# Optimization experiments

Hardware: AMD Instinct MI355X
Metric: run time of the kernel (lower is better)

## Reference

```python
import jax, jax.numpy as jnp
import numpy as np

SLOPE = 25.0  # surrogate gradient slope of ALIFNeuron
EPS = 1e-5    # LayerNorm eps


def spike_fn(u):
    # forward: heaviside(u); backward: sigmoid surrogate with slope SLOPE
    s = jax.nn.sigmoid(SLOPE * u)
    hard = (u > 0).astype(u.dtype)
    return s + jax.lax.stop_gradient(hard - s)


def layernorm(x, w, b):
    mu = jnp.mean(x, axis=-1, keepdims=True)
    var = jnp.mean((x - mu) ** 2, axis=-1, keepdims=True)
    return (x - mu) * jax.lax.rsqrt(var + EPS) * w + b


def setup_inputs() -> dict:
    key = jax.random.key(0)
    k1, k2, k3 = jax.random.split(key, 3)
    B, T, D = 8, 4096, 1024
    num_nodes = 15  # (1 << 4) - 1
    x = jax.random.normal(k1, (B, T, D), dtype=jnp.float32)
    # Linear(2D -> D) weights for each tree node, scaled ~ 1/sqrt(fan_in)
    W = jax.random.normal(k2, (num_nodes, 2 * D, D), dtype=jnp.float32) * 0.02
    b = jnp.zeros((num_nodes, D), dtype=jnp.float32)
    # base_threshold init = 0.5 in torch; use uniform around it
    bt = jax.random.uniform(k3, (num_nodes, D), dtype=jnp.float32)
    ln_w = jnp.ones((D,), dtype=jnp.float32)
    ln_b = jnp.zeros((D,), dtype=jnp.float32)
    return {"x": x, "W": W, "b": b, "bt": bt, "ln_w": ln_w, "ln_b": ln_b}


def reference(x, W, b, bt, ln_w, ln_b):
    # TreeSelfAttentionHybrid._forward_parallel with fresh (zero) ALIF state:
    # v=adapt=0 => ALIF spike = H(proj - base_threshold) with surrogate grad.
    B, T, D = x.shape
    tree_depth = 4
    num_nodes = (1 << tree_depth) - 1          # 15
    eff_depth = tree_depth                     # log2(T) >= tree_depth here
    num_leaves = 1 << eff_depth                # 16
    sub_seq = T // num_leaves
    # leaf pooling: [B, 16, D]
    leaves = x.reshape(B, num_leaves, sub_seq, D).mean(axis=2)
    leaf_start = (1 << (eff_depth - 1)) - 1    # 7
    n_used = num_nodes - leaf_start            # only gids 7..14 fit in tree
    used = leaves[:, :n_used]                  # [B, 8, D]
    fused = jnp.concatenate([used, used], axis=-1)  # [B, 8, 2D]
    proj = jnp.einsum('bnd,nde->bne', fused, W[leaf_start:num_nodes]) + b[leaf_start:num_nodes]
    states = proj * spike_fn(proj - bt[leaf_start:num_nodes])  # [B, 8, D]
    # internal levels: 2 -> 1 -> 0
    for level in range(eff_depth - 2, -1, -1):
        start = (1 << level) - 1
        size = 1 << level
        fused = jnp.concatenate([states[:, 0::2], states[:, 1::2]], axis=-1)  # [B,size,2D]
        proj = jnp.einsum('bnd,nde->bne', fused, W[start:start + size]) + b[start:start + size]
        states = proj * spike_fn(proj - bt[start:start + size])
    root = states[:, 0]                        # [B, D]
    out = root[:, None, :] + x                 # broadcast expand over T
    return layernorm(out, ln_w, ln_b)
```

## Files before the change

### kernel.cpp

```cpp
#include <hip/hip_runtime.h>

#define D 1024
#define NB 8
#define T 4096

typedef float fvec4 __attribute__((ext_vector_type(4)));

__global__ void __launch_bounds__(256) leaves_partial(const float* __restrict__ x,
                                                      float* __restrict__ lpart) {
    int b = blockIdx.x, leaf = blockIdx.y, tc = blockIdx.z;
    int tid = threadIdx.x;
    const float4* xp = (const float4*)x;
    size_t base = ((size_t)b * T + (size_t)leaf * 256 + (size_t)tc * 32) * (D / 4) + tid;
    float4 acc = {0.f, 0.f, 0.f, 0.f};
#pragma unroll 8
    for (int tt = 0; tt < 32; ++tt) {
        float4 v = xp[base + (size_t)tt * (D / 4)];
        acc.x += v.x; acc.y += v.y; acc.z += v.z; acc.w += v.w;
    }
    ((float4*)lpart)[(((b * 8 + leaf) * 8 + tc) * (D / 4)) + tid] = acc;
}

template <int KCH, int KCPREV, int MODE>
__global__ void __launch_bounds__(256) tree_gemm(const float* __restrict__ gprev,
                                                 const float* __restrict__ W,
                                                 const float* __restrict__ bias,
                                                 const float* __restrict__ bt,
                                                 float* __restrict__ gout,
                                                 int node_base, int prev_base) {
    int node = blockIdx.x;
    int c0 = blockIdx.y * 256;
    int k0 = blockIdx.z * KCH;
    int tid = threadIdx.x;
    int nkc = gridDim.z;

    __shared__ float fs[KCH][8];
    for (int idx = tid; idx < KCH * 8; idx += 256) {
        int kk = idx % KCH;
        int b = idx / KCH;
        int k = k0 + kk;
        int col = k & 1023;
        float v;
        if (MODE == 0) {
            float p = 0.f;
#pragma unroll
            for (int tc = 0; tc < 8; ++tc)
                p += gprev[(((size_t)(b * 8 + node)) * 8 + tc) * D + col];
            v = p * (1.0f / 256.0f);
        } else {
            int src = 2 * node + (k >> 10);
            float p = bias[(size_t)(prev_base + src) * D + col];
#pragma unroll
            for (int kc = 0; kc < KCPREV; ++kc)
                p += gprev[(((size_t)src * KCPREV + kc) * 8 + b) * D + col];
            float u = p - bt[(size_t)(prev_base + src) * D + col];
            v = (u > 0.0f) ? p : 0.0f;
        }
        fs[kk][b] = v;
    }
    __syncthreads();

    int col = c0 + tid;
    const float* Wp = W + (size_t)(node_base + node) * 2048 * D + (size_t)k0 * D + col;
    float acc0 = 0.f, acc1 = 0.f, acc2 = 0.f, acc3 = 0.f;
    float acc4 = 0.f, acc5 = 0.f, acc6 = 0.f, acc7 = 0.f;
#pragma unroll 8
    for (int kk = 0; kk < KCH; ++kk) {
        float w = Wp[(size_t)kk * D];
        float4 f0 = *(const float4*)&fs[kk][0];
        float4 f1 = *(const float4*)&fs[kk][4];
        acc0 += f0.x * w; acc1 += f0.y * w; acc2 += f0.z * w; acc3 += f0.w * w;
        acc4 += f1.x * w; acc5 += f1.y * w; acc6 += f1.z * w; acc7 += f1.w * w;
    }
    size_t gb = ((size_t)(node * nkc + blockIdx.z) * 8) * D + col;
    gout[gb + 0 * D] = acc0; gout[gb + 1 * D] = acc1;
    gout[gb + 2 * D] = acc2; gout[gb + 3 * D] = acc3;
    gout[gb + 4 * D] = acc4; gout[gb + 5 * D] = acc5;
    gout[gb + 6 * D] = acc6; gout[gb + 7 * D] = acc7;
}

template <int KC>
__global__ void __launch_bounds__(256) root_gate(const float* __restrict__ gpart,
                                                 const float* __restrict__ bias,
                                                 const float* __restrict__ bt,
                                                 float* __restrict__ root) {
    int gid = blockIdx.x * 256 + threadIdx.x;
    int col = gid & 1023;
    int b = gid >> 10;
    float p = bias[col];
#pragma unroll
    for (int kc = 0; kc < KC; ++kc)
        p += gpart[((size_t)kc * 8 + b) * D + col];
    float u = p - bt[col];
    root[gid] = (u > 0.0f) ? p : 0.0f;
}

__global__ void __launch_bounds__(256) add_ln(const float* __restrict__ x,
                                              const float* __restrict__ root,
                                              const float* __restrict__ lw,
                                              const float* __restrict__ lb,
                                              float* __restrict__ out) {
    int row = blockIdx.x;
    int b = row >> 12;
    int tid = threadIdx.x;
    const fvec4* xr = (const fvec4*)x + (size_t)row * (D / 4);
    float4 r = ((const float4*)root)[b * (D / 4) + tid];
    fvec4 vv = __builtin_nontemporal_load(xr + tid);
    float4 v;
    v.x = vv.x + r.x; v.y = vv.y + r.y; v.z = vv.z + r.z; v.w = vv.w + r.w;

    float s = v.x + v.y + v.z + v.w;
    float q = v.x * v.x + v.y * v.y + v.z * v.z + v.w * v.w;
#pragma unroll
    for (int off = 32; off; off >>= 1) {
        s += __shfl_down(s, off);
        q += __shfl_down(q, off);
    }
    __shared__ float ss[4], sq[4];
    int wave = tid >> 6, lane = tid & 63;
    if (lane == 0) { ss[wave] = s; sq[wave] = q; }
    __syncthreads();
    s = ss[0] + ss[1] + ss[2] + ss[3];
    q = sq[0] + sq[1] + sq[2] + sq[3];

    float mean = s * (1.0f / D);
    float var = q * (1.0f / D) - mean * mean;
    float rstd = rsqrtf(var + 1e-5f);

    float4 w4 = ((const float4*)lw)[tid];
    float4 b4 = ((const float4*)lb)[tid];
    fvec4 o;
    o.x = (v.x - mean) * rstd * w4.x + b4.x;
    o.y = (v.y - mean) * rstd * w4.y + b4.y;
    o.z = (v.z - mean) * rstd * w4.z + b4.z;
    o.w = (v.w - mean) * rstd * w4.w + b4.w;
    __builtin_nontemporal_store(o, (fvec4*)out + (size_t)row * (D / 4) + tid);
}

extern "C" void kernel_launch(void* const* d_in, const int* in_sizes, int n_in,
                              void* d_out, int out_size, void* d_ws, size_t ws_size,
                              hipStream_t stream) {
    const float* x    = (const float*)d_in[0];
    const float* W    = (const float*)d_in[1];
    const float* bias = (const float*)d_in[2];
    const float* bt   = (const float*)d_in[3];
    const float* lw   = (const float*)d_in[4];
    const float* lb   = (const float*)d_in[5];
    float* out = (float*)d_out;

    float* ws    = (float*)d_ws;
    float* lpart = ws;
    float* gA    = lpart + 524288;
    float* gB    = gA + 1048576;
    float* root  = gB + 524288;

    leaves_partial<<<dim3(8, 8, 8), 256, 0, stream>>>(x, lpart);

    tree_gemm<128, 8, 0><<<dim3(8, 4, 16), 256, 0, stream>>>(
        lpart, W, bias, bt, gA, 7, 0);
    tree_gemm<128, 16, 1><<<dim3(4, 4, 16), 256, 0, stream>>>(
        gA, W, bias, bt, gB, 3, 7);
    tree_gemm<64, 16, 1><<<dim3(2, 4, 32), 256, 0, stream>>>(
        gB, W, bias, bt, gA, 1, 3);
    tree_gemm<32, 32, 1><<<dim3(1, 4, 64), 256, 0, stream>>>(
        gA, W, bias, bt, gB, 0, 1);

    root_gate<64><<<32, 256, 0, stream>>>(gB, bias, bt, root);

    add_ln<<<NB * T, 256, 0, stream>>>(x, root, lw, lb, out);
}
```

Measured before the change: 123.1 us.

## Rework tree GEMM tiling, vectorize weights, parallelize root reduction and per-wave LayerNorm

Tree GEMM kernels now have each thread load float4 weights covering all 1024 columns, and the K range is split into many more chunks so every level launches 256 blocks. Weight loads use nontemporal hints and the workspace is enlarged to hold the extra partials. The root gate reduction is spread across 512 blocks with a shared-memory reduction. LayerNorm now handles one row per wave using xor shuffles, with no block barrier. The finer K split means more partial-sum traffic in exchange for better occupancy and wider loads.

After: 108.1 us. 1.14x faster.

```diff
diff --git a/kernel.cpp b/kernel.cpp
--- a/kernel.cpp
+++ b/kernel.cpp
@@ -6,35 +6,34 @@
 
 typedef float fvec4 __attribute__((ext_vector_type(4)));
 
-__global__ void __launch_bounds__(256) leaves_partial(const float* __restrict__ x,
-                                                      float* __restrict__ lpart) {
-    int b = blockIdx.x, leaf = blockIdx.y, tc = blockIdx.z;
+__global__ void __launch_bounds__(256, 2) leaves_partial(const float* __restrict__ x,
+                                                         float* __restrict__ lpart) {
+    int bid = blockIdx.x;
+    int b = bid >> 6, leaf = (bid >> 3) & 7, tc = bid & 7;
     int tid = threadIdx.x;
-    const float4* xp = (const float4*)x;
-    size_t base = ((size_t)b * T + (size_t)leaf * 256 + (size_t)tc * 32) * (D / 4) + tid;
-    float4 acc = {0.f, 0.f, 0.f, 0.f};
+    const fvec4* xp = (const fvec4*)x;
+    size_t base = ((size_t)(b * T + leaf * 256 + tc * 32)) * 256 + tid;
+    fvec4 acc = {0.f, 0.f, 0.f, 0.f};
 #pragma unroll 8
-    for (int tt = 0; tt < 32; ++tt) {
-        float4 v = xp[base + (size_t)tt * (D / 4)];
-        acc.x += v.x; acc.y += v.y; acc.z += v.z; acc.w += v.w;
-    }
-    ((float4*)lpart)[(((b * 8 + leaf) * 8 + tc) * (D / 4)) + tid] = acc;
+    for (int tt = 0; tt < 32; ++tt)
+        acc += xp[base + (size_t)tt * 256];
+    ((fvec4*)lpart)[(size_t)((b * 8 + leaf) * 8 + tc) * 256 + tid] = acc;
 }
 
-template <int KCH, int KCPREV, int MODE>
-__global__ void __launch_bounds__(256) tree_gemm(const float* __restrict__ gprev,
-                                                 const float* __restrict__ W,
-                                                 const float* __restrict__ bias,
-                                                 const float* __restrict__ bt,
-                                                 float* __restrict__ gout,
-                                                 int node_base, int prev_base) {
-    int node = blockIdx.x;
-    int c0 = blockIdx.y * 256;
-    int k0 = blockIdx.z * KCH;
+template <int KCH, int NKC, int KCPREV, int MODE>
+__global__ void __launch_bounds__(256, 2) tree_gemm(const float* __restrict__ gprev,
+                                                    const float* __restrict__ W,
+                                                    const float* __restrict__ bias,
+                                                    const float* __restrict__ bt,
+                                                    float* __restrict__ gout,
+                                                    int node_base, int prev_base) {
+    int bid = blockIdx.x;
+    int node = bid / NKC;
+    int kc = bid % NKC;
+    int k0 = kc * KCH;
     int tid = threadIdx.x;
-    int nkc = gridDim.z;
 
-    __shared__ float fs[KCH][8];
+    __shared__ float fs[KCH * 8];
     for (int idx = tid; idx < KCH * 8; idx += 256) {
         int kk = idx % KCH;
         int b = idx / KCH;
@@ -45,97 +44,109 @@
             float p = 0.f;
 #pragma unroll
             for (int tc = 0; tc < 8; ++tc)
-                p += gprev[(((size_t)(b * 8 + node)) * 8 + tc) * D + col];
+                p += gprev[(size_t)((b * 8 + node) * 8 + tc) * D + col];
             v = p * (1.0f / 256.0f);
         } else {
             int src = 2 * node + (k >> 10);
             float p = bias[(size_t)(prev_base + src) * D + col];
-#pragma unroll
-            for (int kc = 0; kc < KCPREV; ++kc)
-                p += gprev[(((size_t)src * KCPREV + kc) * 8 + b) * D + col];
+#pragma unroll 16
+            for (int kcp = 0; kcp < KCPREV; ++kcp)
+                p += gprev[(size_t)((src * KCPREV + kcp) * 8 + b) * D + col];
             float u = p - bt[(size_t)(prev_base + src) * D + col];
             v = (u > 0.0f) ? p : 0.0f;
         }
-        fs[kk][b] = v;
+        fs[kk * 8 + b] = v;
     }
     __syncthreads();
 
-    int col = c0 + tid;
-    const float* Wp = W + (size_t)(node_base + node) * 2048 * D + (size_t)k0 * D + col;
-    float acc0 = 0.f, acc1 = 0.f, acc2 = 0.f, acc3 = 0.f;
-    float acc4 = 0.f, acc5 = 0.f, acc6 = 0.f, acc7 = 0.f;
-#pragma unroll 8
+    const fvec4* Wp = (const fvec4*)W +
+                      ((size_t)(node_base + node) * 2048 + (size_t)k0) * 256 + tid;
+    fvec4 acc[8];
+#pragma unroll
+    for (int b = 0; b < 8; ++b) acc[b] = (fvec4){0.f, 0.f, 0.f, 0.f};
+#pragma unroll 4
     for (int kk = 0; kk < KCH; ++kk) {
-        float w = Wp[(size_t)kk * D];
-        float4 f0 = *(const float4*)&fs[kk][0];
-        float4 f1 = *(const float4*)&fs[kk][4];
-        acc0 += f0.x * w; acc1 += f0.y * w; acc2 += f0.z * w; acc3 += f0.w * w;
-        acc4 += f1.x * w; acc5 += f1.y * w; acc6 += f1.z * w; acc7 += f1.w * w;
+        fvec4 w = __builtin_nontemporal_load(Wp + (size_t)kk * 256);
+#pragma unroll
+        for (int b = 0; b < 8; ++b) acc[b] += w * fs[kk * 8 + b];
     }
-    size_t gb = ((size_t)(node * nkc + blockIdx.z) * 8) * D + col;
-    gout[gb + 0 * D] = acc0; gout[gb + 1 * D] = acc1;
-    gout[gb + 2 * D] = acc2; gout[gb + 3 * D] = acc3;
-    gout[gb + 4 * D] = acc4; gout[gb + 5 * D] = acc5;
-    gout[gb + 6 * D] = acc6; gout[gb + 7 * D] = acc7;
+    fvec4* op = (fvec4*)gout + (size_t)((node * NKC + kc) * 8) * 256 + tid;
+#pragma unroll
+    for (int b = 0; b < 8; ++b) op[(size_t)b * 256] = acc[b];
 }
 
 template <int KC>
-__global__ void __launch_bounds__(256) root_gate(const float* __restrict__ gpart,
-                                                 const float* __restrict__ bias,
-                                                 const float* __restrict__ bt,
-                                                 float* __restrict__ root) {
-    int gid = blockIdx.x * 256 + threadIdx.x;
-    int col = gid & 1023;
-    int b = gid >> 10;
-    float p = bias[col];
+__global__ void __launch_bounds__(256, 2) root_gate(const float* __restrict__ gpart,
+                                                    const float* __restrict__ bias,
+                                                    const float* __restrict__ bt,
+                                                    float* __restrict__ root) {
+    int b = blockIdx.x >> 6;
+    int colg = blockIdx.x & 63;
+    int tid = threadIdx.x;
+    int c = tid & 15, s = tid >> 4;
+    int col = colg * 16 + c;
+    float p = 0.f;
+#pragma unroll 4
+    for (int kc = s; kc < KC; kc += 16)
+        p += gpart[(size_t)(kc * 8 + b) * D + col];
+    __shared__ float sm[256];
+    sm[s * 16 + c] = p;
+    __syncthreads();
+    if (tid < 16) {
+        int col2 = colg * 16 + tid;
+        float tot = bias[col2];
 #pragma unroll
-    for (int kc = 0; kc < KC; ++kc)
-        p += gpart[((size_t)kc * 8 + b) * D + col];
-    float u = p - bt[col];
-    root[gid] = (u > 0.0f) ? p : 0.0f;
+        for (int ss = 0; ss < 16; ++ss) tot += sm[ss * 16 + tid];
+        float u = tot - bt[col2];
+        root[b * D + col2] = (u > 0.0f) ? tot : 0.0f;
+    }
 }
 
-__global__ void __launch_bounds__(256) add_ln(const float* __restrict__ x,
-                                              const float* __restrict__ root,
-                                              const float* __restrict__ lw,
-                                              const float* __restrict__ lb,
-                                              float* __restrict__ out) {
-    int row = blockIdx.x;
+__global__ void __launch_bounds__(256, 2) add_ln(const float* __restrict__ x,
+                                                 const float* __restrict__ root,
+                                                 const float* __restrict__ lw,
+                                                 const float* __restrict__ lb,
+                                                 float* __restrict__ out) {
+    int tid = threadIdx.x;
+    int wv = tid >> 6, lane = tid & 63;
+    int row = blockIdx.x * 4 + wv;
     int b = row >> 12;
-    int tid = threadIdx.x;
-    const fvec4* xr = (const fvec4*)x + (size_t)row * (D / 4);
-    float4 r = ((const float4*)root)[b * (D / 4) + tid];
-    fvec4 vv = __builtin_nontemporal_load(xr + tid);
-    float4 v;
-    v.x = vv.x + r.x; v.y = vv.y + r.y; v.z = vv.z + r.z; v.w = vv.w + r.w;
+    const fvec4* xp = (const fvec4*)x;
+    const fvec4* rp = (const fvec4*)root + b * 256;
+    const fvec4* lwp = (const fvec4*)lw;
+    const fvec4* lbp = (const fvec4*)lb;
 
-    float s = v.x + v.y + v.z + v.w;
-    float q = v.x * v.x + v.y * v.y + v.z * v.z + v.w * v.w;
+    fvec4 rv[4], lwv[4], lbv[4], v[4];
+#pragma unroll
+    for (int j = 0; j < 4; ++j) {
+        rv[j] = rp[j * 64 + lane];
+        lwv[j] = lwp[j * 64 + lane];
+        lbv[j] = lbp[j * 64 + lane];
+    }
+    float s = 0.f, q = 0.f;
+#pragma unroll
+    for (int j = 0; j < 4; ++j) {
+        fvec4 xv = xp[(size_t)row * 256 + j * 64 + lane];
+        v[j] = xv + rv[j];
+        s += v[j].x + v[j].y + v[j].z + v[j].w;
+        q += v[j].x * v[j].x + v[j].y * v[j].y + v[j].z * v[j].z + v[j].w * v[j].w;
+    }
 #pragma unroll
     for (int off = 32; off; off >>= 1) {
-        s += __shfl_down(s, off);
-        q += __shfl_down(q, off);
+        s += __shfl_xor(s, off);
+        q += __shfl_xor(q, off);
     }
-    __shared__ float ss[4], sq[4];
-    int wave = tid >> 6, lane = tid & 63;
-    if (lane == 0) { ss[wave] = s; sq[wave] = q; }
-    __syncthreads();
-    s = ss[0] + ss[1] + ss[2] + ss[3];
-    q = sq[0] + sq[1] + sq[2] + sq[3];
-
     float mean = s * (1.0f / D);
     float var = q * (1.0f / D) - mean * mean;
     float rstd = rsqrtf(var + 1e-5f);
+    fvec4* op = (fvec4*)out + (size_t)row * 256;
+#pragma unroll
+    for (int j = 0; j < 4; ++j) {
+        fvec4 o = (v[j] - mean) * rstd * lwv[j] + lbv[j];
+        __builtin_nontemporal_store(o, op + j * 64 + lane);
+    }
+}
 
-    float4 w4 = ((const float4*)lw)[tid];
-    float4 b4 = ((const float4*)lb)[tid];
-    fvec4 o;
-    o.x = (v.x - mean) * rstd * w4.x + b4.x;
-    o.y = (v.y - mean) * rstd * w4.y + b4.y;
-    o.z = (v.z - mean) * rstd * w4.z + b4.z;
-    o.w = (v.w - mean) * rstd * w4.w + b4.w;
-    __builtin_nontemporal_store(o, (fvec4*)out + (size_t)row * (D / 4) + tid);
-}
 
 extern "C" void kernel_launch(void* const* d_in, const int* in_sizes, int n_in,
                               void* d_out, int out_size, void* d_ws, size_t ws_size,
@@ -148,24 +159,20 @@
     const float* lb   = (const float*)d_in[5];
     float* out = (float*)d_out;
 
-    float* ws    = (float*)d_ws;
+    float* ws = (float*)d_ws;
     float* lpart = ws;
     float* gA    = lpart + 524288;
-    float* gB    = gA + 1048576;
-    float* root  = gB + 524288;
+    float* gB    = gA + 2097152;
+    float* root  = gB + 2097152;
 
-    leaves_partial<<<dim3(8, 8, 8), 256, 0, stream>>>(x, lpart);
+    leaves_partial<<<512, 256, 0, stream>>>(x, lpart);
 
-    tree_gemm<128, 8, 0><<<dim3(8, 4, 16), 256, 0, stream>>>(
-        lpart, W, bias, bt, gA, 7, 0);
-    tree_gemm<128, 16, 1><<<dim3(4, 4, 16), 256, 0, stream>>>(
-        gA, W, bias, bt, gB, 3, 7);
-    tree_gemm<64, 16, 1><<<dim3(2, 4, 32), 256, 0, stream>>>(
-        gB, W, bias, bt, gA, 1, 3);
-    tree_gemm<32, 32, 1><<<dim3(1, 4, 64), 256, 0, stream>>>(
-        gA, W, bias, bt, gB, 0, 1);
+    tree_gemm<64, 32, 8, 0><<<256, 256, 0, stream>>>(lpart, W, bias, bt, gA, 7, 0);
+    tree_gemm<32, 64, 32, 1><<<256, 256, 0, stream>>>(gA, W, bias, bt, gB, 3, 7);
+    tree_gemm<16, 128, 64, 1><<<256, 256, 0, stream>>>(gB, W, bias, bt, gA, 1, 3);
+    tree_gemm<8, 256, 128, 1><<<256, 256, 0, stream>>>(gA, W, bias, bt, gB, 0, 1);
 
-    root_gate<64><<<32, 256, 0, stream>>>(gB, bias, bt, root);
+    root_gate<256><<<512, 256, 0, stream>>>(gB, bias, bt, root);
 
-    add_ln<<<NB * T, 256, 0, stream>>>(x, root, lw, lb, out);
+    add_ln<<<NB * T / 4, 256, 0, stream>>>(x, root, lw, lb, out);
 }
```
